# Optimization experiments

Measured on AMD Instinct MI355X. Metric: run time of the kernel, lower is better.

The kernel has to match this reference:

```python
import jax, jax.numpy as jnp
import numpy as np
from jax import lax

KSIZE = 7
SIGMA = 5.0
ALPHA = 0.05


def _gaussian_kernel(ksize: int, sigma: float) -> jnp.ndarray:
    # 2D Gaussian, normalized to sum 1, replicated depthwise for 3 channels: (3,1,k,k)
    ax = jnp.arange(ksize, dtype=jnp.float32) - (ksize - 1) / 2.0
    g1 = jnp.exp(-(ax ** 2) / (2.0 * sigma ** 2))
    g2 = jnp.outer(g1, g1)
    g2 = g2 / jnp.sum(g2)
    return jnp.broadcast_to(g2[None, None], (3, 1, ksize, ksize)).astype(jnp.float32)


def _sobel_kernel() -> jnp.ndarray:
    # (2,1,3,3): channel 0 -> Ix, channel 1 -> Iy
    sx = jnp.array([[-1.0, 0.0, 1.0], [-2.0, 0.0, 2.0], [-1.0, 0.0, 1.0]], dtype=jnp.float32)
    sy = sx.T
    return jnp.stack([sx[None], sy[None]], axis=0)  # (2,1,3,3)


def setup_inputs() -> dict:
    key = jax.random.key(0)
    x = jax.random.normal(key, (1, 1, 4096, 4096), dtype=jnp.float32)
    return {"x": x, "sobel_k": _sobel_kernel(), "gauss_k": _gaussian_kernel(KSIZE, SIGMA)}


def _conv(x, k, pad, groups):
    return lax.conv_general_dilated(
        x, k, window_strides=(1, 1), padding=[(pad, pad), (pad, pad)],
        dimension_numbers=("NCHW", "OIHW", "NCHW"), feature_group_count=groups)


def reference(x, sobel_k, gauss_k):
    # ImageGradientsLayer: Sobel conv -> (1,2,H,W)
    g = _conv(x, sobel_k, 1, 1)
    Ix, Iy = g[:, 0:1], g[:, 1:2]
    # ChannelProductLayer -> (1,3,H,W)
    prod = jnp.concatenate([Ix * Ix, Iy * Iy, Ix * Iy], axis=1)
    # SecondMomentMatrixLayer: depthwise Gaussian blur, groups=3
    S = _conv(prod, gauss_k, KSIZE // 2, 3)
    Sxx, Syy, Sxy = S[0, 0], S[0, 1], S[0, 2]
    # CornerResponseLayer: R = det - alpha*trace^2
    tr = Sxx + Syy
    R = (Sxx * Syy - Sxy * Sxy - ALPHA * tr * tr)[None, None]  # (1,1,H,W)
    # NMSLayer: median threshold, 7x7 maxpool (stride 1, pad 3), keep maxima
    med = jnp.median(R)
    Rt = jnp.where(R >= med, R, jnp.float32(0.0))
    mp = lax.reduce_window(Rt, -jnp.inf, lax.max, (1, 1, 7, 7), (1, 1, 1, 1),
                           [(0, 0), (0, 0), (3, 3), (3, 3)])
    out = jnp.where(Rt != mp, jnp.float32(0.0), mp)
    return out
```

## Files before the change

kernel.cpp:

```cpp
#include <hip/hip_runtime.h>
#include <math.h>

#define N_IMG 4096
#define NBC   1024
#define H_OUT 32
#define HR    38
#define NPIX  (N_IMG * N_IMG)
#define HBLK  1024

struct W7 { float w[7]; };

__device__ __forceinline__ unsigned f2k(float f) {
    unsigned u = __float_as_uint(f);
    return (u & 0x80000000u) ? ~u : (u | 0x80000000u);
}
__device__ __forceinline__ float k2f(unsigned k) {
    unsigned u = (k & 0x80000000u) ? (k & 0x7fffffffu) : ~k;
    return __uint_as_float(u);
}

struct SelState { unsigned p1, p2, r1, r2; };

template<int BINS>
__device__ void locate_pair(const unsigned* h0, const unsigned* h1,
                            int shift, SelState& s)
{
    __shared__ unsigned scan[256];
    __shared__ unsigned resb[2], resr[2];
    const int tid = threadIdx.x;
    const int per = BINS / 256;
    const bool same = (h0 == h1);

    for (int q = 0; q < 2; q++) {
        if (q == 1 && same) break;
        const unsigned* h = q ? h1 : h0;
        const int base = tid * per;
        unsigned sum = 0;
        #pragma unroll
        for (int i = 0; i < per; i++) sum += h[base + i];
        __syncthreads();
        scan[tid] = sum;
        __syncthreads();
        unsigned v = sum;
        #pragma unroll
        for (int off = 1; off < 256; off <<= 1) {
            unsigned t = (tid >= off) ? scan[tid - off] : 0u;
            __syncthreads();
            v += t;
            scan[tid] = v;
            __syncthreads();
        }
        const unsigned excl = v - sum;
        #pragma unroll
        for (int w = 0; w < 2; w++) {
            const unsigned rank = w ? s.r2 : s.r1;
            const bool mine = w ? (same || q == 1) : (q == 0);
            if (mine && rank >= excl && rank < v) {
                unsigned rr = rank - excl;
                for (int i = 0; i < per; i++) {
                    unsigned c = h[base + i];
                    if (rr < c) { resb[w] = (unsigned)(base + i); resr[w] = rr; break; }
                    rr -= c;
                }
            }
        }
        __syncthreads();
    }
    s.p1 |= resb[0] << shift; s.r1 = resr[0];
    s.p2 |= resb[1] << shift; s.r2 = resr[1];
}

__device__ __forceinline__ SelState derive0(const unsigned* g0) {
    SelState s; s.p1 = 0u; s.p2 = 0u;
    s.r1 = (unsigned)(NPIX / 2 - 1); s.r2 = (unsigned)(NPIX / 2);
    locate_pair<4096>(g0, g0, 20, s);
    return s;
}
__device__ __forceinline__ void derive1(const unsigned* g1, SelState& s) {
    const unsigned* h1 = (s.p1 != s.p2) ? (g1 + 4096) : g1;
    locate_pair<4096>(g1, h1, 8, s);
}
__device__ __forceinline__ void derive2(const unsigned* g2, SelState& s) {
    const unsigned* h1 = (s.p1 != s.p2) ? (g2 + 256) : g2;
    locate_pair<256>(g2, h1, 0, s);
}

__global__ __launch_bounds__(256, 2) void harris_kernel(const float* __restrict__ x,
                                                        float* __restrict__ R,
                                                        unsigned* __restrict__ g0,
                                                        W7 wp)
{
    __shared__ unsigned histo[4096];
    const int tid = threadIdx.x;
    for (int i = tid; i < 4096; i += 256) histo[i] = 0;
    __syncthreads();

    const int row0 = blockIdx.y * H_OUT;
    const int jc   = blockIdx.x * NBC + tid * 4;
    const float* w = wp.w;
    const bool edge = (jc < 4) || (jc >= N_IMG - 8);

    float xm[12], xc[12], xp[12], xn[12];
    float axx[7][4], ayy[7][4], axy[7][4];

    #pragma unroll
    for (int m = 0; m < 7; m++)
        #pragma unroll
        for (int o = 0; o < 4; o++) { axx[m][o] = 0.f; ayy[m][o] = 0.f; axy[m][o] = 0.f; }

    auto loadrow = [&](int ri, float* d) {
        if ((unsigned)ri < N_IMG) {
            const float* p = x + (size_t)ri * N_IMG;
            float4 v0 = make_float4(0.f,0.f,0.f,0.f), v2 = make_float4(0.f,0.f,0.f,0.f);
            if (jc >= 4) v0 = *(const float4*)(p + jc - 4);
            float4 v1 = *(const float4*)(p + jc);
            if (jc + 4 < N_IMG) v2 = *(const float4*)(p + jc + 4);
            d[0]=v0.x; d[1]=v0.y; d[2]=v0.z; d[3]=v0.w;
            d[4]=v1.x; d[5]=v1.y; d[6]=v1.z; d[7]=v1.w;
            d[8]=v2.x; d[9]=v2.y; d[10]=v2.z; d[11]=v2.w;
        } else {
            #pragma unroll
            for (int t = 0; t < 12; t++) d[t] = 0.f;
        }
    };

    loadrow(row0 - 4, xm);
    loadrow(row0 - 3, xc);
    loadrow(row0 - 2, xp);

    int curb = -1; unsigned cnt = 0;

    auto step = [&](int r, int k, int dmin, bool emit) {
        const int ri = row0 + r - 3;
        loadrow(ri + 2, xn);

        if ((unsigned)ri < N_IMG) {
            float dc[12], rd[12];
            #pragma unroll
            for (int t = 0; t < 12; t++) {
                dc[t] = xm[t] + 2.f * xc[t] + xp[t];
                rd[t] = xp[t] - xm[t];
            }
            float ixv[10], iyv[10];
            #pragma unroll
            for (int t = 0; t < 10; t++) {
                ixv[t] = dc[t+2] - dc[t];
                iyv[t] = rd[t] + 2.f * rd[t+1] + rd[t+2];
            }
            if (edge) {
                #pragma unroll
                for (int t = 0; t < 10; t++)
                    if ((unsigned)(jc - 3 + t) >= N_IMG) { ixv[t] = 0.f; iyv[t] = 0.f; }
            }
            float sxx[4] = {0,0,0,0}, syy[4] = {0,0,0,0}, sxy[4] = {0,0,0,0};
            #pragma unroll
            for (int t = 0; t < 10; t++) {
                float ix = ixv[t], iy = iyv[t];
                float xx = ix*ix, yy = iy*iy, xy = ix*iy;
                #pragma unroll
                for (int o = 0; o < 4; o++) {
                    const int v = t - o;
                    if (v >= 0 && v < 7) {
                        sxx[o] = fmaf(w[v], xx, sxx[o]);
                        syy[o] = fmaf(w[v], yy, syy[o]);
                        sxy[o] = fmaf(w[v], xy, sxy[o]);
                    }
                }
            }
            #pragma unroll
            for (int d = 0; d < 7; d++) {
                if (d >= dmin) {
                    const int m = (k + d) % 7;
                    #pragma unroll
                    for (int o = 0; o < 4; o++) {
                        axx[m][o] = fmaf(w[6-d], sxx[o], axx[m][o]);
                        ayy[m][o] = fmaf(w[6-d], syy[o], ayy[m][o]);
                        axy[m][o] = fmaf(w[6-d], sxy[o], axy[m][o]);
                    }
                }
            }
        }

        if (emit) {
            float4 h;
            float* hp = &h.x;
            #pragma unroll
            for (int o = 0; o < 4; o++) {
                float ax = axx[k][o], ay = ayy[k][o], az = axy[k][o];
                axx[k][o] = 0.f; ayy[k][o] = 0.f; axy[k][o] = 0.f;
                float tr = ax + ay;
                hp[o] = ax*ay - az*az - 0.05f*tr*tr;
            }
            const int orow = row0 + r - 6;
            *(float4*)(R + (size_t)orow * N_IMG + jc) = h;
            #pragma unroll
            for (int o = 0; o < 4; o++) {
                int b = (int)(f2k(hp[o]) >> 20);
                if (b == curb) cnt++;
                else { if (curb >= 0) atomicAdd(&histo[curb], cnt); curb = b; cnt = 1; }
            }
        }
        #pragma unroll
        for (int t = 0; t < 12; t++) { xm[t] = xc[t]; xc[t] = xp[t]; xp[t] = xn[t]; }
    };

    #pragma unroll
    for (int rr = 0; rr < 7; ++rr)
        step(rr, rr, 6 - rr, rr == 6);
    for (int it = 1; it < 6; ++it) {
        #pragma unroll
        for (int k = 0; k < 7; ++k) {
            const int r = it * 7 + k;
            if (r < HR) step(r, k, 0, true);
        }
    }

    if (curb >= 0) atomicAdd(&histo[curb], cnt);
    __syncthreads();
    for (int i = tid; i < 4096; i += 256) {
        unsigned c = histo[i];
        if (c) atomicAdd(&g0[i], c);
    }
}

__global__ __launch_bounds__(256) void hist1_kernel(const float* __restrict__ R,
                                                    const unsigned* __restrict__ g0,
                                                    unsigned* __restrict__ g1)
{
    __shared__ unsigned h[2][4096];
    const int tid = threadIdx.x;
    for (int i = tid; i < 8192; i += 256) ((unsigned*)h)[i] = 0u;

    SelState s = derive0(g0);
    const unsigned p1 = s.p1, p2 = s.p2;
    const bool dual = (p1 != p2);
    const unsigned mask = 0xFFF00000u;
    const int shift = 8;

    const int n4 = NPIX / 4;
    const int stride = gridDim.x * 256;
    int curb1 = -1; unsigned cnt1 = 0;
    int curb2 = -1; unsigned cnt2 = 0;
    const float4* R4 = (const float4*)R;

    auto proc = [&](unsigned k) {
        if ((k & mask) == p1) {
            int b = (int)((k >> shift) & 4095u);
            if (b == curb1) cnt1++;
            else { if (cnt1) atomicAdd(&h[0][curb1], cnt1); curb1 = b; cnt1 = 1; }
        }
        if (dual && (k & mask) == p2) {
            int b = (int)((k >> shift) & 4095u);
            if (b == curb2) cnt2++;
            else { if (cnt2) atomicAdd(&h[1][curb2], cnt2); curb2 = b; cnt2 = 1; }
        }
    };

    int i = blockIdx.x * 256 + tid;
    for (; i + 3 * stride < n4; i += 4 * stride) {
        float4 va = R4[i];
        float4 vb = R4[i + stride];
        float4 vc = R4[i + 2 * stride];
        float4 vd = R4[i + 3 * stride];
        float vv[16] = {va.x, va.y, va.z, va.w, vb.x, vb.y, vb.z, vb.w,
                        vc.x, vc.y, vc.z, vc.w, vd.x, vd.y, vd.z, vd.w};
        #pragma unroll
        for (int t = 0; t < 16; t++) proc(f2k(vv[t]));
    }
    for (; i < n4; i += stride) {
        float4 va = R4[i];
        float vv[4] = {va.x, va.y, va.z, va.w};
        #pragma unroll
        for (int t = 0; t < 4; t++) proc(f2k(vv[t]));
    }
    if (cnt1) atomicAdd(&h[0][curb1], cnt1);
    if (cnt2) atomicAdd(&h[1][curb2], cnt2);
    __syncthreads();
    for (int j = tid; j < 4096; j += 256) {
        unsigned c0 = h[0][j]; if (c0) atomicAdd(&g1[j], c0);
        if (dual) { unsigned c1 = h[1][j]; if (c1) atomicAdd(&g1[4096 + j], c1); }
    }
}

__global__ __launch_bounds__(256) void hist2_kernel(const float* __restrict__ R,
                                                    const unsigned* __restrict__ g0,
                                                    const unsigned* __restrict__ g1,
                                                    unsigned* __restrict__ g2)
{
    __shared__ unsigned h[2][256];
    const int tid = threadIdx.x;
    for (int i = tid; i < 512; i += 256) ((unsigned*)h)[i] = 0u;

    SelState s = derive0(g0);
    derive1(g1, s);
    const unsigned p1 = s.p1, p2 = s.p2;
    const bool dual = (p1 != p2);
    const unsigned mask = 0xFFFFFF00u;

    const int n4 = NPIX / 4;
    const int stride = gridDim.x * 256;
    int curb1 = -1; unsigned cnt1 = 0;
    int curb2 = -1; unsigned cnt2 = 0;
    const float4* R4 = (const float4*)R;

    auto proc = [&](unsigned k) {
        if ((k & mask) == p1) {
            int b = (int)(k & 255u);
            if (b == curb1) cnt1++;
            else { if (cnt1) atomicAdd(&h[0][curb1], cnt1); curb1 = b; cnt1 = 1; }
        }
        if (dual && (k & mask) == p2) {
            int b = (int)(k & 255u);
            if (b == curb2) cnt2++;
            else { if (cnt2) atomicAdd(&h[1][curb2], cnt2); curb2 = b; cnt2 = 1; }
        }
    };

    int i = blockIdx.x * 256 + tid;
    for (; i + 3 * stride < n4; i += 4 * stride) {
        float4 va = R4[i];
        float4 vb = R4[i + stride];
        float4 vc = R4[i + 2 * stride];
        float4 vd = R4[i + 3 * stride];
        float vv[16] = {va.x, va.y, va.z, va.w, vb.x, vb.y, vb.z, vb.w,
                        vc.x, vc.y, vc.z, vc.w, vd.x, vd.y, vd.z, vd.w};
        #pragma unroll
        for (int t = 0; t < 16; t++) proc(f2k(vv[t]));
    }
    for (; i < n4; i += stride) {
        float4 va = R4[i];
        float vv[4] = {va.x, va.y, va.z, va.w};
        #pragma unroll
        for (int t = 0; t < 4; t++) proc(f2k(vv[t]));
    }
    if (cnt1) atomicAdd(&h[0][curb1], cnt1);
    if (cnt2) atomicAdd(&h[1][curb2], cnt2);
    __syncthreads();
    if (tid < 256) {
        unsigned c0 = h[0][tid]; if (c0) atomicAdd(&g2[tid], c0);
        if (dual) { unsigned c1 = h[1][tid]; if (c1) atomicAdd(&g2[256 + tid], c1); }
    }
}

__global__ __launch_bounds__(256) void init_kernel(unsigned* __restrict__ g)
{
    const int tid = threadIdx.x;
    for (int i = tid; i < 12800; i += 256) g[i] = 0u;
}

__global__ __launch_bounds__(256, 2) void nms_kernel(const float* __restrict__ R,
                                                     const unsigned* __restrict__ g0,
                                                     const unsigned* __restrict__ g1,
                                                     const unsigned* __restrict__ g2,
                                                     float* __restrict__ out)
{
    const int tid  = threadIdx.x;

    SelState s = derive0(g0);
    derive1(g1, s);
    derive2(g2, s);
    const float med = 0.5f * (k2f(s.p1) + k2f(s.p2));

    const int row0 = blockIdx.y * H_OUT;
    const int jc   = blockIdx.x * NBC + tid * 4;

    float vm[7][4];
    float ct[7][4];
    #pragma unroll
    for (int m = 0; m < 7; m++)
        #pragma unroll
        for (int o = 0; o < 4; o++) vm[m][o] = -INFINITY;

    auto loadrowT = [&](int ri, float* d) {
        if ((unsigned)ri < N_IMG) {
            const float* p = R + (size_t)ri * N_IMG;
            float4 v1 = *(const float4*)(p + jc);
            d[4] = (v1.x >= med) ? v1.x : 0.f;
            d[5] = (v1.y >= med) ? v1.y : 0.f;
            d[6] = (v1.z >= med) ? v1.z : 0.f;
            d[7] = (v1.w >= med) ? v1.w : 0.f;
            if (jc >= 4) {
                float4 v0 = *(const float4*)(p + jc - 4);
                d[0] = (v0.x >= med) ? v0.x : 0.f;
                d[1] = (v0.y >= med) ? v0.y : 0.f;
                d[2] = (v0.z >= med) ? v0.z : 0.f;
                d[3] = (v0.w >= med) ? v0.w : 0.f;
            } else { d[0]=d[1]=d[2]=d[3] = -INFINITY; }
            if (jc + 4 < N_IMG) {
                float4 v2 = *(const float4*)(p + jc + 4);
                d[8]  = (v2.x >= med) ? v2.x : 0.f;
                d[9]  = (v2.y >= med) ? v2.y : 0.f;
                d[10] = (v2.z >= med) ? v2.z : 0.f;
                d[11] = (v2.w >= med) ? v2.w : 0.f;
            } else { d[8]=d[9]=d[10]=d[11] = -INFINITY; }
        } else {
            #pragma unroll
            for (int t = 0; t < 12; t++) d[t] = -INFINITY;
        }
    };

    auto stepn = [&](int r, int k, int dmin, bool emit) {
        const int ri = row0 + r - 3;
        float a[12];
        loadrowT(ri, a);
        float hm[4];
        #pragma unroll
        for (int o = 0; o < 4; o++) {
            float m01 = fmaxf(a[o+1], a[o+2]);
            float m23 = fmaxf(a[o+3], a[o+4]);
            float m45 = fmaxf(a[o+5], a[o+6]);
            hm[o] = fmaxf(fmaxf(m01, m23), fmaxf(m45, a[o+7]));
            ct[k][o] = a[4+o];
        }
        #pragma unroll
        for (int d = 0; d < 7; d++) {
            if (d >= dmin) {
                const int m = (k + d) % 7;
                #pragma unroll
                for (int o = 0; o < 4; o++)
                    vm[m][o] = fmaxf(vm[m][o], hm[o]);
            }
        }
        if (emit) {
            float4 ov;
            float* op = &ov.x;
            #pragma unroll
            for (int o = 0; o < 4; o++) {
                float m = vm[k][o];
                vm[k][o] = -INFINITY;
                float c = ct[(k+4) % 7][o];
                op[o] = (c != m) ? 0.f : m;
            }
            const int orow = row0 + r - 6;
            *(float4*)(out + (size_t)orow * N_IMG + jc) = ov;
        }
    };

    #pragma unroll
    for (int rr = 0; rr < 7; ++rr)
        stepn(rr, rr, 6 - rr, rr == 6);
    for (int it = 1; it < 6; ++it) {
        #pragma unroll
        for (int k = 0; k < 7; ++k) {
            const int r = it * 7 + k;
            if (r < HR) stepn(r, k, 0, true);
        }
    }
}

extern "C" void kernel_launch(void* const* d_in, const int* in_sizes, int n_in,
                              void* d_out, int out_size, void* d_ws, size_t ws_size,
                              hipStream_t stream)
{
    const float* x = (const float*)d_in[0];
    float* R = (float*)d_ws;
    unsigned* g0 = (unsigned*)((char*)d_ws + (size_t)NPIX * 4);
    unsigned* g1 = g0 + 4096;
    unsigned* g2 = g1 + 8192;
    float* out = (float*)d_out;

    W7 wp;
    {
        double g[7], sm = 0.0;
        for (int i = 0; i < 7; i++) { double ax = (double)i - 3.0; g[i] = exp(-(ax*ax)/50.0); sm += g[i]; }
        for (int i = 0; i < 7; i++) wp.w[i] = (float)(g[i] / sm);
    }

    dim3 sgrid(N_IMG / NBC, N_IMG / H_OUT);

    init_kernel<<<1, 256, 0, stream>>>(g0);
    harris_kernel<<<sgrid, 256, 0, stream>>>(x, R, g0, wp);
    hist1_kernel<<<HBLK, 256, 0, stream>>>(R, g0, g1);
    hist2_kernel<<<HBLK, 256, 0, stream>>>(R, g0, g1, g2);
    nms_kernel<<<sgrid, 256, 0, stream>>>(R, g0, g1, g2, out);
}
```

Before: 269.5 us.

## Replace two-pass radix median refinement with single fine histogram pass

The median selection drops the two extra full passes over R (hist1 and hist2) in favour of one pass. That pass either builds a 2^20-bin global fine histogram for the median's top-12-bit bucket, or, when the two middle elements fall in different buckets, reduces a max/min across them. A small kernel then builds a coarse 4096-bin histogram from the fine one, and NMS derives the exact median from these. The aim is to save one full 64MB read of R. In exchange it adds a 4MB histogram zeroing, scattered global atomics and a new path that depends on workspace size.

```diff
diff --git a/kernel.cpp b/kernel.cpp
--- a/kernel.cpp
+++ b/kernel.cpp
@@ -7,6 +7,7 @@
 #define HR    38
 #define NPIX  (N_IMG * N_IMG)
 #define HBLK  1024
+#define FINE_WORDS (1u << 20)
 
 struct W7 { float w[7]; };
 
@@ -83,6 +84,14 @@
 __device__ __forceinline__ void derive2(const unsigned* g2, SelState& s) {
     const unsigned* h1 = (s.p1 != s.p2) ? (g2 + 256) : g2;
     locate_pair<256>(g2, h1, 0, s);
+}
+__device__ __forceinline__ void derive_coarse(const unsigned* coarse, SelState& s) {
+    locate_pair<4096>(coarse, coarse, 8, s);
+}
+__device__ __forceinline__ void derive_fine(const unsigned* fine, SelState& s) {
+    const unsigned* f1 = fine + (((s.p1 >> 8) & 0xFFFu) << 8);
+    const unsigned* f2 = fine + (((s.p2 >> 8) & 0xFFFu) << 8);
+    locate_pair<256>(f1, f2, 0, s);
 }
 
 __global__ __launch_bounds__(256, 2) void harris_kernel(const float* __restrict__ x,
@@ -223,6 +232,75 @@
     }
 }
 
+__global__ __launch_bounds__(256) void histF_kernel(const float* __restrict__ R,
+                                                    const unsigned* __restrict__ g0,
+                                                    unsigned* __restrict__ fine,
+                                                    unsigned* __restrict__ mm)
+{
+    __shared__ unsigned rmax[256], rmin[256];
+    SelState s = derive0(g0);
+    const unsigned p1 = s.p1, p2 = s.p2;
+    const bool dual = (p1 != p2);
+    const unsigned mask = 0xFFF00000u;
+    const int tid = threadIdx.x;
+    const int n4 = NPIX / 4;
+    const float4* R4 = (const float4*)R;
+
+    if (!dual) {
+        unsigned curlo = 0xFFFFFFFFu; unsigned cnt = 0;
+        for (int i = blockIdx.x * 256 + tid; i < n4; i += gridDim.x * 256) {
+            float4 v = R4[i];
+            float vv[4] = {v.x, v.y, v.z, v.w};
+            #pragma unroll
+            for (int t = 0; t < 4; t++) {
+                unsigned k = f2k(vv[t]);
+                if ((k & mask) == p1) {
+                    unsigned lo = k & 0xFFFFFu;
+                    if (lo == curlo) cnt++;
+                    else { if (cnt) atomicAdd(&fine[curlo], cnt); curlo = lo; cnt = 1; }
+                }
+            }
+        }
+        if (cnt) atomicAdd(&fine[curlo], cnt);
+    } else {
+        unsigned bmax = 0u, bmin = 0xFFFFFFFFu;
+        for (int i = blockIdx.x * 256 + tid; i < n4; i += gridDim.x * 256) {
+            float4 v = R4[i];
+            float vv[4] = {v.x, v.y, v.z, v.w};
+            #pragma unroll
+            for (int t = 0; t < 4; t++) {
+                unsigned k = f2k(vv[t]);
+                if ((k & mask) == p1) bmax = max(bmax, k);
+                if ((k & mask) == p2) bmin = min(bmin, k);
+            }
+        }
+        rmax[tid] = bmax; rmin[tid] = bmin;
+        __syncthreads();
+        for (int off = 128; off; off >>= 1) {
+            if (tid < off) {
+                rmax[tid] = max(rmax[tid], rmax[tid + off]);
+                rmin[tid] = min(rmin[tid], rmin[tid + off]);
+            }
+            __syncthreads();
+        }
+        if (tid == 0) { atomicMax(&mm[0], rmax[0]); atomicMin(&mm[1], rmin[0]); }
+    }
+}
+
+__global__ __launch_bounds__(256) void build_coarse_kernel(const unsigned* __restrict__ fine,
+                                                           unsigned* __restrict__ coarse)
+{
+    const int tid = threadIdx.x;
+    const int wave = tid >> 6, lane = tid & 63;
+    const int c = blockIdx.x * 4 + wave;
+    const uint4* f4 = (const uint4*)(fine + (size_t)c * 256);
+    uint4 v = f4[lane];
+    unsigned sm = v.x + v.y + v.z + v.w;
+    #pragma unroll
+    for (int off = 32; off; off >>= 1) sm += __shfl_down(sm, off);
+    if (lane == 0) coarse[c] = sm;
+}
+
 __global__ __launch_bounds__(256) void hist1_kernel(const float* __restrict__ R,
                                                     const unsigned* __restrict__ g0,
                                                     unsigned* __restrict__ g1)
@@ -342,24 +420,45 @@
     }
 }
 
-__global__ __launch_bounds__(256) void init_kernel(unsigned* __restrict__ g)
-{
-    const int tid = threadIdx.x;
-    for (int i = tid; i < 12800; i += 256) g[i] = 0u;
+__global__ __launch_bounds__(256) void init_kernel(unsigned* __restrict__ g,
+                                                   unsigned nwords,
+                                                   unsigned* __restrict__ mm,
+                                                   int fine_mode)
+{
+    for (unsigned i = blockIdx.x * 256u + threadIdx.x; i < nwords; i += gridDim.x * 256u)
+        g[i] = 0u;
+    if (fine_mode && blockIdx.x == 0 && threadIdx.x == 0) {
+        mm[0] = 0u; mm[1] = 0xFFFFFFFFu;
+    }
 }
 
 __global__ __launch_bounds__(256, 2) void nms_kernel(const float* __restrict__ R,
                                                      const unsigned* __restrict__ g0,
                                                      const unsigned* __restrict__ g1,
                                                      const unsigned* __restrict__ g2,
+                                                     const unsigned* __restrict__ coarse,
+                                                     const unsigned* __restrict__ fine,
+                                                     const unsigned* __restrict__ mm,
+                                                     int mode,
                                                      float* __restrict__ out)
 {
     const int tid  = threadIdx.x;
 
     SelState s = derive0(g0);
-    derive1(g1, s);
-    derive2(g2, s);
-    const float med = 0.5f * (k2f(s.p1) + k2f(s.p2));
+    float med;
+    if (mode == 1) {
+        if (s.p1 != s.p2) {
+            med = 0.5f * (k2f(mm[0]) + k2f(mm[1]));
+        } else {
+            derive_coarse(coarse, s);
+            derive_fine(fine, s);
+            med = 0.5f * (k2f(s.p1) + k2f(s.p2));
+        }
+    } else {
+        derive1(g1, s);
+        derive2(g2, s);
+        med = 0.5f * (k2f(s.p1) + k2f(s.p2));
+    }
 
     const int row0 = blockIdx.y * H_OUT;
     const int jc   = blockIdx.x * NBC + tid * 4;
@@ -455,8 +554,6 @@
     const float* x = (const float*)d_in[0];
     float* R = (float*)d_ws;
     unsigned* g0 = (unsigned*)((char*)d_ws + (size_t)NPIX * 4);
-    unsigned* g1 = g0 + 4096;
-    unsigned* g2 = g1 + 8192;
     float* out = (float*)d_out;
 
     W7 wp;
@@ -468,9 +565,27 @@
 
     dim3 sgrid(N_IMG / NBC, N_IMG / H_OUT);
 
-    init_kernel<<<1, 256, 0, stream>>>(g0);
-    harris_kernel<<<sgrid, 256, 0, stream>>>(x, R, g0, wp);
-    hist1_kernel<<<HBLK, 256, 0, stream>>>(R, g0, g1);
-    hist2_kernel<<<HBLK, 256, 0, stream>>>(R, g0, g1, g2);
-    nms_kernel<<<sgrid, 256, 0, stream>>>(R, g0, g1, g2, out);
-}
+    const unsigned fine_words = 4096u + 4096u + 64u + FINE_WORDS;
+    const size_t need_fine = (size_t)NPIX * 4 + (size_t)fine_words * 4;
+
+    if (ws_size >= need_fine) {
+        unsigned* coarse = g0 + 4096;
+        unsigned* mm     = coarse + 4096;
+        unsigned* fine   = mm + 64;
+        init_kernel<<<1024, 256, 0, stream>>>(g0, fine_words, mm, 1);
+        harris_kernel<<<sgrid, 256, 0, stream>>>(x, R, g0, wp);
+        histF_kernel<<<2048, 256, 0, stream>>>(R, g0, fine, mm);
+        build_coarse_kernel<<<1024, 256, 0, stream>>>(fine, coarse);
+        nms_kernel<<<sgrid, 256, 0, stream>>>(R, g0, nullptr, nullptr,
+                                              coarse, fine, mm, 1, out);
+    } else {
+        unsigned* g1 = g0 + 4096;
+        unsigned* g2 = g1 + 8192;
+        init_kernel<<<64, 256, 0, stream>>>(g0, 12800u, nullptr, 0);
+        harris_kernel<<<sgrid, 256, 0, stream>>>(x, R, g0, wp);
+        hist1_kernel<<<HBLK, 256, 0, stream>>>(R, g0, g1);
+        hist2_kernel<<<HBLK, 256, 0, stream>>>(R, g0, g1, g2);
+        nms_kernel<<<sgrid, 256, 0, stream>>>(R, g0, g1, g2,
+                                              nullptr, nullptr, nullptr, 0, out);
+    }
+}
```

New measurement: 262.3 us. 2.7% less time.
